# Performance work log

Measured on AMD Instinct MI355X. Metric: run time of the kernel, lower is better.

The kernel has to match this reference:

```python
import jax, jax.numpy as jnp
import numpy as np

WS = 8  # window size (8,8); num_token n = 64


def setup_inputs() -> dict:
    key = jax.random.key(0)
    ks = jax.random.split(key, 10)
    dim = 28        # channels c
    d = 28          # dim_head
    rank = 28       # sq_dim
    n = WS * WS     # tokens per window
    x = jax.random.normal(ks[0], (1, 8, 256, 256, dim), jnp.float32)

    def lin(k, shape, fan_in):
        return jax.random.normal(k, shape, jnp.float32) / np.sqrt(fan_in).astype(np.float32)

    return {
        "x": x,
        "W_qk": lin(ks[1], (2 * rank, dim), dim),   # to_qk (no bias)
        "W_v": lin(ks[2], (dim, dim), dim),         # to_v (no bias)
        "W_out": lin(ks[3], (dim, dim), dim),       # to_out weight
        "b_out": jnp.zeros((dim,), jnp.float32),    # to_out bias
        "W_pcq": lin(ks[4], (1, d), d),             # pc_proj_q
        "b_pcq": jnp.ones((1,), jnp.float32),       # bias_pc_proj_q (init 1.0)
        "W_pck": lin(ks[5], (1, d), d),             # pc_proj_k
        "b_pck": jnp.ones((1,), jnp.float32),
        "W_m1": lin(ks[6], (1, n), n),              # mlp1: Linear(64,1)
        "W_m2a": lin(ks[7], (n, n), n),             # mlp2: Linear(64,64)
        "W_m2b": lin(ks[8], (1, n), n),             # mlp2: Linear(64,1)
    }


def _fa_forward(x, W_qk, W_v, W_out, b_out, W_pcq, b_pcq, W_pck, b_pck, W_m1, W_m2a, W_m2b):
    b, B, H, Wd, c = x.shape
    nh, nw = H // WS, Wd // WS
    n = WS * WS
    heads = 1  # dim_head == dim == sq_dim -> heads_qk = heads_v = 1
    # window partition: 'b B (h b0) (w b1) c -> (b h w) (b0 b1) B c'
    xw = (x.reshape(b, B, nh, WS, nw, WS, c)
           .transpose(0, 2, 4, 3, 5, 1, 6)
           .reshape(b * nh * nw, n, B, c))
    qk = xw @ W_qk.T                      # [w, n, B, 2*rank]
    q, k = jnp.split(qk, 2, axis=-1)
    v = xw @ W_v.T

    def split_heads(t):                   # [w, n, B, h*d] -> [w, h, B, n, d]
        w_, n_, B_, _ = t.shape
        return t.reshape(w_, n_, B_, heads, -1).transpose(0, 3, 2, 1, 4)

    q, k, v = split_heads(q), split_heads(k), split_heads(v)

    # learned sigma per token
    sig_q = q @ W_pcq.T + b_pcq           # [w, h, B, n, 1]
    sig_k = k @ W_pck.T + b_pck
    sim = jnp.einsum('whBid,whBjd->whBij', q, k)          # raw scores
    Sigma = sig_q * jnp.swapaxes(sig_k, -1, -2)           # outer product [.., i, j]
    # diagonal removal: sim - diag_embed(diag(sim)) == zero the diagonal
    eye = jnp.eye(n, dtype=sim.dtype)
    sim_norm = sim * (1.0 - eye)
    # MLP threshold
    theta = jnp.einsum('whBij,j->whBi', sim_norm, W_m1[0])  # mlp1 over j, squeeze
    t = theta @ W_m2a.T
    t = jnp.where(t >= 0, t, 0.1 * t)                       # LeakyReLU(0.1)
    theta = (t @ W_m2b.T)[..., None]                        # [w, h, B, 1, 1]
    sim = sim * Sigma
    attn = jax.nn.softmax(sim, axis=-1) * (sim > theta).astype(sim.dtype)
    out = jnp.einsum('whBij,whBjd->whBid', attn, v)
    # merge heads: [w, h, B, n, d] -> [w, n, B, h*d]
    out = out.transpose(0, 3, 2, 1, 4).reshape(b * nh * nw, n, B, c)
    out = out @ W_out.T + b_out
    # un-window: '(b h w) (b0 b1) B c -> b B (h b0) (w b1) c'
    out = (out.reshape(b, nh, nw, WS, WS, B, c)
              .transpose(0, 5, 1, 3, 2, 4, 6)
              .reshape(b, B, H, Wd, c))
    return out


def reference(x, W_qk, W_v, W_out, b_out, W_pcq, b_pcq, W_pck, b_pck, W_m1, W_m2a, W_m2b):
    return _fa_forward(x, W_qk, W_v, W_out, b_out, W_pcq, b_pcq,
                       W_pck, b_pck, W_m1, W_m2a, W_m2b)
```

## Files before the change

### kernel.cpp

```cpp
#include <hip/hip_runtime.h>
#include <math.h>

#define C 28
#define N 64

#define A_OFF   0
#define QT_OFF  0
#define KT_OFF  1792
#define V_OFF   2048
#define SQ_OFF  3840
#define SGK_OFF 3904
#define TH_OFF  3968
#define LDS_FLOATS 4032

__global__ __launch_bounds__(128, 2)
void fa_tiled(const float* __restrict__ x,
              const float* __restrict__ Wqk,
              const float* __restrict__ Wv,
              const float* __restrict__ Wout,
              const float* __restrict__ bout,
              const float* __restrict__ Wpcq,
              const float* __restrict__ bpcq,
              const float* __restrict__ Wpck,
              const float* __restrict__ bpck,
              const float* __restrict__ Wm1,
              const float* __restrict__ Wm2a,
              const float* __restrict__ Wm2b,
              float* __restrict__ out)
{
    __shared__ float S[LDS_FLOATS];

    const int tid = threadIdx.x;
    const int wv  = tid >> 6;
    const int ln  = tid & 63;
    const int pid = blockIdx.x;
    const int win = pid >> 3;
    const int Bi  = pid & 7;
    const int hw = win >> 5, ww = win & 31;
    const int b0 = ln >> 3, b1 = ln & 7;
    const size_t base = ((((size_t)Bi * 256) + (size_t)(hw * 8 + b0)) * 256
                         + (size_t)(ww * 8 + b1)) * C;

    const int ti = tid >> 3;
    const int tj = tid & 7;
    const int rg = ti & 7;
    const int gb = ln & 56;

    float vv[16];

    {
        float xr[C];
        {
            const float4* p = (const float4*)(x + base);
            #pragma unroll
            for (int i = 0; i < 7; ++i) {
                float4 t = p[i];
                xr[4*i+0] = t.x; xr[4*i+1] = t.y; xr[4*i+2] = t.z; xr[4*i+3] = t.w;
            }
        }

        if (wv == 0) {
            float sqa0 = 0.f, sqa1 = 0.f;
            #pragma unroll 2
            for (int d4 = 0; d4 < 7; ++d4) {
                float qq[4];
                #pragma unroll
                for (int t = 0; t < 4; ++t) {
                    const int d = 4*d4 + t;
                    float a0 = 0.f, a1 = 0.f;
                    #pragma unroll
                    for (int c = 0; c < C; c += 2) {
                        a0 += Wqk[d*C + c]     * xr[c];
                        a1 += Wqk[d*C + c + 1] * xr[c+1];
                    }
                    qq[t] = a0 + a1;
                    S[QT_OFF + d*64 + ln] = qq[t];
                }
                sqa0 += qq[0] * Wpcq[4*d4+0];
                sqa1 += qq[1] * Wpcq[4*d4+1];
                sqa0 += qq[2] * Wpcq[4*d4+2];
                sqa1 += qq[3] * Wpcq[4*d4+3];
            }
            S[SQ_OFF + ln] = sqa0 + sqa1 + bpcq[0];
            #pragma unroll
            for (int d4 = 0; d4 < 4; ++d4) {
                #pragma unroll
                for (int t = 0; t < 4; ++t) {
                    const int d = 4*d4 + t;
                    float v0 = 0.f, v1 = 0.f;
                    #pragma unroll
                    for (int c = 0; c < C; c += 2) {
                        v0 += Wv[d*C + c]     * xr[c];
                        v1 += Wv[d*C + c + 1] * xr[c+1];
                    }
                    vv[4*d4+t] = v0 + v1;
                }
            }
        } else {
            float ak = 0.f;
            #pragma unroll 2
            for (int d4 = 0; d4 < 7; ++d4) {
                float kk[4];
                #pragma unroll
                for (int t = 0; t < 4; ++t) {
                    const int d = 4*d4 + t;
                    float k0 = 0.f, k1 = 0.f;
                    #pragma unroll
                    for (int c = 0; c < C; c += 2) {
                        k0 += Wqk[(C+d)*C + c]     * xr[c];
                        k1 += Wqk[(C+d)*C + c + 1] * xr[c+1];
                    }
                    kk[t] = k0 + k1;
                    S[KT_OFF + d*64 + ln] = kk[t];
                }
                ak += kk[0] * Wpck[4*d4+0];
                ak += kk[1] * Wpck[4*d4+1];
                ak += kk[2] * Wpck[4*d4+2];
                ak += kk[3] * Wpck[4*d4+3];
            }
            S[SGK_OFF + ln] = ak + bpck[0];
            #pragma unroll
            for (int d4 = 4; d4 < 7; ++d4) {
                #pragma unroll
                for (int t = 0; t < 4; ++t) {
                    const int d = 4*d4 + t;
                    float v0 = 0.f, v1 = 0.f;
                    #pragma unroll
                    for (int c = 0; c < C; c += 2) {
                        v0 += Wv[d*C + c]     * xr[c];
                        v1 += Wv[d*C + c + 1] * xr[c+1];
                    }
                    vv[4*(d4-4)+t] = v0 + v1;
                }
            }
        }
    }
    __syncthreads();

    float acc[8][4];
    #pragma unroll
    for (int cc = 0; cc < 8; ++cc)
        #pragma unroll
        for (int rr = 0; rr < 4; ++rr) acc[cc][rr] = 0.f;

    #pragma unroll 2
    for (int d = 0; d < C; ++d) {
        float4 qa = *(const float4*)&S[QT_OFF + d*64 + 4*ti];
        float4 ka = *(const float4*)&S[KT_OFF + d*64 + 8*tj];
        float4 kb = *(const float4*)&S[KT_OFF + d*64 + 8*tj + 4];
        float q4[4] = {qa.x,qa.y,qa.z,qa.w};
        float k8[8] = {ka.x,ka.y,ka.z,ka.w,kb.x,kb.y,kb.z,kb.w};
        #pragma unroll
        for (int cc = 0; cc < 8; ++cc)
            #pragma unroll
            for (int rr = 0; rr < 4; ++rr)
                acc[cc][rr] += q4[rr] * k8[cc];
    }

    {
        float4 wa = *(const float4*)&Wm1[8*tj];
        float4 wb = *(const float4*)&Wm1[8*tj + 4];
        float w8[8] = {wa.x,wa.y,wa.z,wa.w,wb.x,wb.y,wb.z,wb.w};
        const bool e0 = (4*ti == 8*tj);
        const bool e4 = (4*ti - 8*tj == 4);
        float th4[4];
        #pragma unroll
        for (int rr = 0; rr < 4; ++rr) {
            float s = 0.f;
            #pragma unroll
            for (int cc = 0; cc < 8; ++cc) {
                float term = acc[cc][rr] * w8[cc];
                if (cc == rr     && e0) term = 0.f;
                if (cc == rr + 4 && e4) term = 0.f;
                s += term;
            }
            float tot = 0.f;
            #pragma unroll
            for (int t = 0; t < 8; ++t) tot += __shfl(s, gb + t, 64);
            th4[rr] = tot;
        }
        #pragma unroll
        for (int r = 0; r < 4; ++r)
            if (tj == r) S[TH_OFF + 4*ti + r] = th4[r];
    }
    __syncthreads();

    if (wv == 0) {
        *(float4*)&S[V_OFF + ln*C +  0] = make_float4(vv[0], vv[1], vv[2], vv[3]);
        *(float4*)&S[V_OFF + ln*C +  4] = make_float4(vv[4], vv[5], vv[6], vv[7]);
        *(float4*)&S[V_OFF + ln*C +  8] = make_float4(vv[8], vv[9], vv[10],vv[11]);
        *(float4*)&S[V_OFF + ln*C + 12] = make_float4(vv[12],vv[13],vv[14],vv[15]);
    } else {
        *(float4*)&S[V_OFF + ln*C + 16] = make_float4(vv[0], vv[1], vv[2], vv[3]);
        *(float4*)&S[V_OFF + ln*C + 20] = make_float4(vv[4], vv[5], vv[6], vv[7]);
        *(float4*)&S[V_OFF + ln*C + 24] = make_float4(vv[8], vv[9], vv[10],vv[11]);
    }

    float theta;
    {
        const float* wrow = Wm2a + ln * N;
        float a0 = 0.f, a1 = 0.f, a2 = 0.f, a3 = 0.f;
        #pragma unroll 4
        for (int i4 = 0; i4 < 16; ++i4) {
            float4 t4 = *(const float4*)&S[TH_OFF + 4*i4];
            float4 w4 = *(const float4*)&wrow[4*i4];
            a0 += t4.x*w4.x; a1 += t4.y*w4.y; a2 += t4.z*w4.z; a3 += t4.w*w4.w;
        }
        float t = (a0 + a1) + (a2 + a3);
        t = (t >= 0.f) ? t : 0.1f * t;
        theta = t * Wm2b[ln];
        #pragma unroll
        for (int off = 32; off > 0; off >>= 1)
            theta += __shfl_xor(theta, off, 64);
    }

    {
        float4 a = *(const float4*)&S[SQ_OFF + 4*ti];
        float sq4[4] = {a.x, a.y, a.z, a.w};
        float4 c0 = *(const float4*)&S[SGK_OFF + 8*tj];
        float4 c1 = *(const float4*)&S[SGK_OFF + 8*tj + 4];
        float sg8[8] = {c0.x,c0.y,c0.z,c0.w,c1.x,c1.y,c1.z,c1.w};
        #pragma unroll
        for (int cc = 0; cc < 8; ++cc)
            #pragma unroll
            for (int rr = 0; rr < 4; ++rr)
                acc[cc][rr] = (acc[cc][rr] * sq4[rr]) * sg8[cc];
    }

    float m4[4];
    #pragma unroll
    for (int rr = 0; rr < 4; ++rr) {
        float mp = -1e30f;
        #pragma unroll
        for (int cc = 0; cc < 8; ++cc) mp = fmaxf(mp, acc[cc][rr]);
        #pragma unroll
        for (int off = 1; off < 8; off <<= 1)
            mp = fmaxf(mp, __shfl_xor(mp, off, 64));
        m4[rr] = mp;
    }

    float z4[4];
    #pragma unroll
    for (int rr = 0; rr < 4; ++rr) {
        float zp = 0.f;
        #pragma unroll
        for (int cc = 0; cc < 8; ++cc) {
            float ss = acc[cc][rr];
            float e = __expf(ss - m4[rr]);
            zp += e;
            acc[cc][rr] = (ss > theta) ? e : 0.f;
        }
        float z = 0.f;
        #pragma unroll
        for (int t = 0; t < 8; ++t) z += __shfl(zp, gb + t, 64);
        z4[rr] = z;
    }

    float* Aw = &S[A_OFF + 1024*wv];
    if ((tj >> 2) == 0) {
        #pragma unroll
        for (int cc = 0; cc < 8; ++cc) {
            const int jl = 8*(tj & 3) + cc;
            *(float4*)&Aw[jl*32 + ((4*rg + 4*(jl & 7)) & 31)] =
                make_float4(acc[cc][0], acc[cc][1], acc[cc][2], acc[cc][3]);
        }
    }
    __syncthreads();

    const int dg  = tj;
    const int dgc = (dg < 7) ? dg : 6;
    float pav0[4] = {0,0,0,0}, pav1[4] = {0,0,0,0};
    float pav2[4] = {0,0,0,0}, pav3[4] = {0,0,0,0};

    #pragma unroll 8
    for (int jl = 0; jl < 32; ++jl) {
        float4 a4 = *(const float4*)&Aw[jl*32 + ((4*rg + 4*(jl & 7)) & 31)];
        float4 v4 = *(const float4*)&S[V_OFF + jl*C + 4*dgc];
        pav0[0] += a4.x*v4.x; pav0[1] += a4.x*v4.y; pav0[2] += a4.x*v4.z; pav0[3] += a4.x*v4.w;
        pav1[0] += a4.y*v4.x; pav1[1] += a4.y*v4.y; pav1[2] += a4.y*v4.z; pav1[3] += a4.y*v4.w;
        pav2[0] += a4.z*v4.x; pav2[1] += a4.z*v4.y; pav2[2] += a4.z*v4.z; pav2[3] += a4.z*v4.w;
        pav3[0] += a4.w*v4.x; pav3[1] += a4.w*v4.y; pav3[2] += a4.w*v4.z; pav3[3] += a4.w*v4.w;
    }

    if ((tj >> 2) == 1) {
        #pragma unroll
        for (int cc = 0; cc < 8; ++cc) {
            const int jl = 8*(tj & 3) + cc;
            *(float4*)&Aw[jl*32 + ((4*rg + 4*(jl & 7)) & 31)] =
                make_float4(acc[cc][0], acc[cc][1], acc[cc][2], acc[cc][3]);
        }
    }

    #pragma unroll 8
    for (int jl = 0; jl < 32; ++jl) {
        float4 a4 = *(const float4*)&Aw[jl*32 + ((4*rg + 4*(jl & 7)) & 31)];
        float4 v4 = *(const float4*)&S[V_OFF + (32 + jl)*C + 4*dgc];
        pav0[0] += a4.x*v4.x; pav0[1] += a4.x*v4.y; pav0[2] += a4.x*v4.z; pav0[3] += a4.x*v4.w;
        pav1[0] += a4.y*v4.x; pav1[1] += a4.y*v4.y; pav1[2] += a4.y*v4.z; pav1[3] += a4.y*v4.w;
        pav2[0] += a4.z*v4.x; pav2[1] += a4.z*v4.y; pav2[2] += a4.z*v4.z; pav2[3] += a4.z*v4.w;
        pav3[0] += a4.w*v4.x; pav3[1] += a4.w*v4.y; pav3[2] += a4.w*v4.z; pav3[3] += a4.w*v4.w;
    }

    {
        float rz0 = 1.0f / z4[0], rz1 = 1.0f / z4[1];
        float rz2 = 1.0f / z4[2], rz3 = 1.0f / z4[3];
        #pragma unroll
        for (int t = 0; t < 4; ++t) {
            pav0[t] *= rz0; pav1[t] *= rz1; pav2[t] *= rz2; pav3[t] *= rz3;
        }
    }

    if (dg < 7) {
        *(float4*)&Aw[(4*rg+0)*C + 4*dg] = make_float4(pav0[0],pav0[1],pav0[2],pav0[3]);
        *(float4*)&Aw[(4*rg+1)*C + 4*dg] = make_float4(pav1[0],pav1[1],pav1[2],pav1[3]);
        *(float4*)&Aw[(4*rg+2)*C + 4*dg] = make_float4(pav2[0],pav2[1],pav2[2],pav2[3]);
        *(float4*)&Aw[(4*rg+3)*C + 4*dg] = make_float4(pav3[0],pav3[1],pav3[2],pav3[3]);
    }
    __syncthreads();

    float o[C];
    {
        const float* orow = &S[A_OFF + 1024*(ln >> 5) + (ln & 31)*C];
        #pragma unroll
        for (int i = 0; i < 7; ++i) {
            float4 t = *(const float4*)(orow + 4*i);
            o[4*i+0] = t.x; o[4*i+1] = t.y; o[4*i+2] = t.z; o[4*i+3] = t.w;
        }
    }
    if (wv == 0) {
        float y[16];
        #pragma unroll 2
        for (int e4 = 0; e4 < 4; ++e4) {
            #pragma unroll
            for (int t = 0; t < 4; ++t) {
                const int e = 4*e4 + t;
                float a0 = 0.f, a1 = 0.f;
                #pragma unroll
                for (int d = 0; d < C; d += 2) {
                    a0 += Wout[e*C + d]     * o[d];
                    a1 += Wout[e*C + d + 1] * o[d+1];
                }
                y[e] = (a0 + a1) + bout[e];
            }
        }
        float4* yp = (float4*)(out + base);
        #pragma unroll
        for (int i = 0; i < 4; ++i)
            yp[i] = make_float4(y[4*i+0], y[4*i+1], y[4*i+2], y[4*i+3]);
    } else {
        float y[12];
        #pragma unroll 2
        for (int e4 = 0; e4 < 3; ++e4) {
            #pragma unroll
            for (int t = 0; t < 4; ++t) {
                const int e = 16 + 4*e4 + t;
                float a0 = 0.f, a1 = 0.f;
                #pragma unroll
                for (int d = 0; d < C; d += 2) {
                    a0 += Wout[e*C + d]     * o[d];
                    a1 += Wout[e*C + d + 1] * o[d+1];
                }
                y[4*e4+t] = (a0 + a1) + bout[e];
            }
        }
        float4* yp = (float4*)(out + base + 16);
        #pragma unroll
        for (int i = 0; i < 3; ++i)
            yp[i] = make_float4(y[4*i+0], y[4*i+1], y[4*i+2], y[4*i+3]);
    }
}

extern "C" void kernel_launch(void* const* d_in, const int* in_sizes, int n_in,
                              void* d_out, int out_size, void* d_ws, size_t ws_size,
                              hipStream_t stream) {
    const float* x     = (const float*)d_in[0];
    const float* W_qk  = (const float*)d_in[1];
    const float* W_v   = (const float*)d_in[2];
    const float* W_out = (const float*)d_in[3];
    const float* b_out = (const float*)d_in[4];
    const float* W_pcq = (const float*)d_in[5];
    const float* b_pcq = (const float*)d_in[6];
    const float* W_pck = (const float*)d_in[7];
    const float* b_pck = (const float*)d_in[8];
    const float* W_m1  = (const float*)d_in[9];
    const float* W_m2a = (const float*)d_in[10];
    const float* W_m2b = (const float*)d_in[11];
    float* y = (float*)d_out;

    hipLaunchKernelGGL(fa_tiled, dim3(8192), dim3(128), 0, stream,
                       x, W_qk, W_v, W_out, b_out, W_pcq, b_pcq,
                       W_pck, b_pck, W_m1, W_m2a, W_m2b, y);
}
```

Baseline: 228.6 us.

## Use DPP row-shift prefix sums for 8-lane reductions, retune LDS swizzle and occupancy

Replaces the 8-step __shfl gather-sum used for theta and softmax denominators with a 7-step DPP row_shr prefix scan, taking the total from the last lane of each group. Theta is then stored with one float4 write from lane tj==7. The attention-tile LDS swizzle changes from jl&7 to jl>>3, and launch bounds move to 4 blocks per SM. The aim is to cut ds_bpermute traffic and raise occupancy, at the risk of register spills and of DPP row shifts not matching the 8-lane group layout.

```diff
diff --git a/kernel.cpp b/kernel.cpp
--- a/kernel.cpp
+++ b/kernel.cpp
@@ -13,7 +13,18 @@
 #define TH_OFF  3968
 #define LDS_FLOATS 4032
 
-__global__ __launch_bounds__(128, 2)
+__device__ __forceinline__ float prefix8_asc(float s) {
+    float p = s;
+    #pragma unroll
+    for (int k = 0; k < 7; ++k) {
+        int sh = __builtin_amdgcn_update_dpp(0, __float_as_int(p),
+                                             0x111 , 0xF, 0xF, true);
+        p = __int_as_float(sh) + s;
+    }
+    return p;
+}
+
+__global__ __launch_bounds__(128, 4)
 void fa_tiled(const float* __restrict__ x,
               const float* __restrict__ Wqk,
               const float* __restrict__ Wv,
@@ -174,14 +185,11 @@
                 if (cc == rr + 4 && e4) term = 0.f;
                 s += term;
             }
-            float tot = 0.f;
-            #pragma unroll
-            for (int t = 0; t < 8; ++t) tot += __shfl(s, gb + t, 64);
-            th4[rr] = tot;
-        }
-        #pragma unroll
-        for (int r = 0; r < 4; ++r)
-            if (tj == r) S[TH_OFF + 4*ti + r] = th4[r];
+            th4[rr] = prefix8_asc(s);
+        }
+        if (tj == 7)
+            *(float4*)&S[TH_OFF + 4*ti] =
+                make_float4(th4[0], th4[1], th4[2], th4[3]);
     }
     __syncthreads();
 
@@ -250,10 +258,8 @@
             zp += e;
             acc[cc][rr] = (ss > theta) ? e : 0.f;
         }
-        float z = 0.f;
-        #pragma unroll
-        for (int t = 0; t < 8; ++t) z += __shfl(zp, gb + t, 64);
-        z4[rr] = z;
+        float zpre = prefix8_asc(zp);
+        z4[rr] = __shfl(zpre, gb + 7, 64);
     }
 
     float* Aw = &S[A_OFF + 1024*wv];
@@ -261,7 +267,7 @@
         #pragma unroll
         for (int cc = 0; cc < 8; ++cc) {
             const int jl = 8*(tj & 3) + cc;
-            *(float4*)&Aw[jl*32 + ((4*rg + 4*(jl & 7)) & 31)] =
+            *(float4*)&Aw[jl*32 + ((4*rg + 4*(jl >> 3)) & 31)] =
                 make_float4(acc[cc][0], acc[cc][1], acc[cc][2], acc[cc][3]);
         }
     }
@@ -274,7 +280,7 @@
 
     #pragma unroll 8
     for (int jl = 0; jl < 32; ++jl) {
-        float4 a4 = *(const float4*)&Aw[jl*32 + ((4*rg + 4*(jl & 7)) & 31)];
+        float4 a4 = *(const float4*)&Aw[jl*32 + ((4*rg + 4*(jl >> 3)) & 31)];
         float4 v4 = *(const float4*)&S[V_OFF + jl*C + 4*dgc];
         pav0[0] += a4.x*v4.x; pav0[1] += a4.x*v4.y; pav0[2] += a4.x*v4.z; pav0[3] += a4.x*v4.w;
         pav1[0] += a4.y*v4.x; pav1[1] += a4.y*v4.y; pav1[2] += a4.y*v4.z; pav1[3] += a4.y*v4.w;
@@ -286,14 +292,14 @@
         #pragma unroll
         for (int cc = 0; cc < 8; ++cc) {
             const int jl = 8*(tj & 3) + cc;
-            *(float4*)&Aw[jl*32 + ((4*rg + 4*(jl & 7)) & 31)] =
+            *(float4*)&Aw[jl*32 + ((4*rg + 4*(jl >> 3)) & 31)] =
                 make_float4(acc[cc][0], acc[cc][1], acc[cc][2], acc[cc][3]);
         }
     }
 
     #pragma unroll 8
     for (int jl = 0; jl < 32; ++jl) {
-        float4 a4 = *(const float4*)&Aw[jl*32 + ((4*rg + 4*(jl & 7)) & 31)];
+        float4 a4 = *(const float4*)&Aw[jl*32 + ((4*rg + 4*(jl >> 3)) & 31)];
         float4 v4 = *(const float4*)&S[V_OFF + (32 + jl)*C + 4*dgc];
         pav0[0] += a4.x*v4.x; pav0[1] += a4.x*v4.y; pav0[2] += a4.x*v4.z; pav0[3] += a4.x*v4.w;
         pav1[0] += a4.y*v4.x; pav1[1] += a4.y*v4.y; pav1[2] += a4.y*v4.z; pav1[3] += a4.y*v4.w;
```

New measurement: 224.2 us. No clear change (-1.9%).
